# Kernel tuning notes

Measured on AMD Instinct MI355X. Metric: run time of the kernel, lower is better.

The kernel has to match this reference:

```python
import jax, jax.numpy as jnp
import numpy as np

B, C, N, K = 8, 256, 16384, 128  # batch, channels, points per cloud, clusters per cloud


def setup_inputs() -> dict:
    key = jax.random.key(0)
    k1, k2 = jax.random.split(key)
    point_features = jax.random.normal(k1, (B, C, N), dtype=jnp.float32)
    # labels in [-1, K): -1 = noise (skipped by the reduce)
    cluster_ids = jax.random.randint(k2, (B, N), 0, K + 1).astype(jnp.int32) - 1
    return {"point_features": point_features, "cluster_ids": cluster_ids}


def reference(point_features, cluster_ids):
    """Faithful vectorized form of SegHead.forward (eval mode: dropout p=0.3 is identity).

    The torch code loops over (pc, unique cluster label) and does a max over each
    ragged segment. With dense labels 0..K-1 this is exactly a segment-max over
    global segment id pc*K + label; label -1 points are routed to a dump segment.
    """
    b_idx = jnp.arange(B, dtype=cluster_ids.dtype)[:, None]                 # (B,1)
    seg = jnp.where(cluster_ids >= 0, b_idx * K + cluster_ids, B * K)       # (B,N)
    feats = point_features.transpose(0, 2, 1).reshape(B * N, C)             # (B*N, C)
    seg_max = jax.ops.segment_max(feats, seg.reshape(-1), num_segments=B * K + 1)
    all_seg_feats = seg_max[: B * K]                                        # (B*K, C)
    # guard vacuously-empty segments (-inf) -> 0, keeps shapes static under jit
    all_seg_feats = jnp.where(jnp.isfinite(all_seg_feats), all_seg_feats, 0.0)
    # point_features permuted + flattened, as the module writes back
    pf_flat = point_features.transpose(0, 2, 1).reshape(-1, C)              # (B*N, C)
    return all_seg_feats, pf_flat
```

## Files before the change

### kernel.cpp

```cpp
#include <hip/hip_runtime.h>
#include <stdint.h>

#define B_ 8
#define C_ 256
#define N_ 16384
#define K_ 128

#define CT 64
#define PT 1024
#define SUB 64
#define NSUB (PT / SUB)
#define TPAD 65

__device__ __forceinline__ unsigned f2key(float f) {
    unsigned u = __float_as_uint(f);
    return (u & 0x80000000u) ? ~u : (u | 0x80000000u);
}
__device__ __forceinline__ float key2f(unsigned k) {
    unsigned u = (k & 0x80000000u) ? (k & 0x7fffffffu) : ~k;
    return __uint_as_float(u);
}

__global__ __launch_bounds__(256, 2) void seghead_fused(
    const float* __restrict__ pf,
    const int* __restrict__ cid,
    unsigned* __restrict__ gacc,
    float* __restrict__ out1)
{
    __shared__ float tile[CT][TPAD];
    __shared__ unsigned acc[K_ * CT];
    __shared__ int cids[PT];

    const int t = threadIdx.x;
    const int b = blockIdx.z;
    const int c0 = blockIdx.y * CT;
    const int n0 = blockIdx.x * PT;

    for (int i = t; i < K_ * CT; i += 256) acc[i] = 0u;
    for (int i = t; i < PT; i += 256) cids[i] = cid[b * N_ + n0 + i];
    __syncthreads();

    const int x4   = t & 15;
    const int cy   = t >> 4;
    const int lane = t & 63;
    const int w    = t >> 6;

    for (int s = 0; s < NSUB; ++s) {
        const int nb = n0 + s * SUB;

        const float* src = pf + ((size_t)b * C_ + c0) * N_ + nb;
        #pragma unroll
        for (int r = 0; r < 4; ++r) {
            const int c = r * 16 + cy;
            float4 v = *(const float4*)(src + (size_t)c * N_ + x4 * 4);
            tile[c][x4 * 4 + 0] = v.x;
            tile[c][x4 * 4 + 1] = v.y;
            tile[c][x4 * 4 + 2] = v.z;
            tile[c][x4 * 4 + 3] = v.w;
        }
        __syncthreads();

        #pragma unroll
        for (int q = 0; q < 16; ++q) {
            const int nl = w * 16 + q;
            const float v = tile[lane][nl];
            out1[((size_t)b * N_ + nb + nl) * C_ + c0 + lane] = v;
            const int cc = cids[s * SUB + nl];
            if (cc >= 0) atomicMax(&acc[cc * CT + lane], f2key(v));
        }
        __syncthreads();
    }

    for (int i = t; i < K_ * CT; i += 256) {
        const unsigned k = acc[i];
        if (k) {
            const int cl = i >> 6;
            const int ch = i & (CT - 1);
            atomicMax(&gacc[(size_t)(b * K_ + cl) * C_ + c0 + ch], k);
        }
    }
}

__global__ void seghead_finalize(unsigned* __restrict__ gacc) {
    const int i = blockIdx.x * 256 + threadIdx.x;
    const unsigned k = gacc[i];
    ((float*)gacc)[i] = k ? key2f(k) : 0.0f;
}

extern "C" void kernel_launch(void* const* d_in, const int* in_sizes, int n_in,
                              void* d_out, int out_size, void* d_ws, size_t ws_size,
                              hipStream_t stream) {
    const float* pf  = (const float*)d_in[0];
    const int*   cid = (const int*)d_in[1];

    float*    out  = (float*)d_out;
    unsigned* gacc = (unsigned*)d_out;
    float*    out1 = out + (size_t)B_ * K_ * C_;

    hipMemsetAsync(d_out, 0, (size_t)B_ * K_ * C_ * sizeof(unsigned), stream);

    dim3 grid(N_ / PT, C_ / CT, B_);
    seghead_fused<<<grid, 256, 0, stream>>>(pf, cid, gacc, out1);

    seghead_finalize<<<(B_ * K_ * C_) / 256, 256, 0, stream>>>(gacc);
}
```

Baseline: 261.1 us.

## Double-buffer tiles, shrink channel tile, stage atomics at load, reduce partials via workspace

Halves the channel tile to 32 so each block uses less LDS and more blocks fit per CU. Adds a double-buffered shared tile with register prefetch of the next sub-tile, and moves the shared atomicMax into the staging step, using a padded [channel][cluster] accumulator. The transposed output is now written as float4. When the workspace is large enough, per-block partial maxima go to the workspace and a separate kernel reduces them deterministically, which removes the global atomics and the memset at the cost of extra workspace traffic.

```diff
diff --git a/kernel.cpp b/kernel.cpp
--- a/kernel.cpp
+++ b/kernel.cpp
@@ -6,11 +6,15 @@
 #define N_ 16384
 #define K_ 128
 
-#define CT 64
+#define CT 32
 #define PT 1024
 #define SUB 64
 #define NSUB (PT / SUB)
-#define TPAD 65
+#define XBLKS (N_ / PT)
+#define YBLKS (C_ / CT)
+#define ACC_ENTRIES (CT * K_)
+#define NBLOCKS (XBLKS * YBLKS * B_)
+#define WS_BYTES ((size_t)NBLOCKS * ACC_ENTRIES * 4u)
 
 __device__ __forceinline__ unsigned f2key(float f) {
     unsigned u = __float_as_uint(f);
@@ -21,67 +25,109 @@
     return __uint_as_float(u);
 }
 
-__global__ __launch_bounds__(256, 2) void seghead_fused(
+__global__ __launch_bounds__(256, 4) void seghead_fused(
     const float* __restrict__ pf,
     const int* __restrict__ cid,
-    unsigned* __restrict__ gacc,
-    float* __restrict__ out1)
+    float* __restrict__ out1,
+    unsigned* __restrict__ pws,
+    unsigned* __restrict__ gacc)
 {
-    __shared__ float tile[CT][TPAD];
-    __shared__ unsigned acc[K_ * CT];
-    __shared__ int cids[PT];
+    __shared__ float tile[2][CT][SUB + 1];
+    __shared__ unsigned acc[CT][K_ + 1];
 
-    const int t = threadIdx.x;
-    const int b = blockIdx.z;
-    const int c0 = blockIdx.y * CT;
-    const int n0 = blockIdx.x * PT;
+    const int t  = threadIdx.x;
+    const int xb = blockIdx.x, yb = blockIdx.y, b = blockIdx.z;
+    const int c0 = yb * CT;
+    const int n0 = xb * PT;
 
-    for (int i = t; i < K_ * CT; i += 256) acc[i] = 0u;
-    for (int i = t; i < PT; i += 256) cids[i] = cid[b * N_ + n0 + i];
+    for (int i = t; i < CT * (K_ + 1); i += 256) ((unsigned*)acc)[i] = 0u;
+
+    const int x4 = t & 15;
+    const int cy = t >> 4;
+    const float* src0 = pf + ((size_t)(b * C_ + c0 + cy) * N_) + n0 + x4 * 4;
+    const int*   csrc = cid + (size_t)b * N_ + n0 + x4 * 4;
+
+    auto gload = [&](int r, int s) -> float4 {
+        return *(const float4*)(src0 + (size_t)r * 16 * N_ + s * SUB);
+    };
+    auto cload = [&](int s) -> int4 {
+        return *(const int4*)(csrc + s * SUB);
+    };
+    auto stage = [&](int nb, float4 v0, float4 v1, int4 cc) {
+        float* row0 = &tile[nb][cy][x4 * 4];
+        float* row1 = &tile[nb][16 + cy][x4 * 4];
+        row0[0] = v0.x; row0[1] = v0.y; row0[2] = v0.z; row0[3] = v0.w;
+        row1[0] = v1.x; row1[1] = v1.y; row1[2] = v1.z; row1[3] = v1.w;
+        if (cc.x >= 0) { atomicMax(&acc[cy][cc.x], f2key(v0.x)); atomicMax(&acc[16 + cy][cc.x], f2key(v1.x)); }
+        if (cc.y >= 0) { atomicMax(&acc[cy][cc.y], f2key(v0.y)); atomicMax(&acc[16 + cy][cc.y], f2key(v1.y)); }
+        if (cc.z >= 0) { atomicMax(&acc[cy][cc.z], f2key(v0.z)); atomicMax(&acc[16 + cy][cc.z], f2key(v1.z)); }
+        if (cc.w >= 0) { atomicMax(&acc[cy][cc.w], f2key(v0.w)); atomicMax(&acc[16 + cy][cc.w], f2key(v1.w)); }
+    };
+
+    const int lane = t & 63;
+    const int w    = t >> 6;
+    const int g4   = (lane & 7) * 4;
+    const int pp   = lane >> 3;
+    auto process = [&](int nb, int s) {
+        #pragma unroll
+        for (int it = 0; it < 2; ++it) {
+            const int p = w * 16 + it * 8 + pp;
+            float4 o;
+            o.x = tile[nb][g4 + 0][p];
+            o.y = tile[nb][g4 + 1][p];
+            o.z = tile[nb][g4 + 2][p];
+            o.w = tile[nb][g4 + 3][p];
+            *(float4*)&out1[((size_t)b * N_ + n0 + s * SUB + p) * C_ + c0 + g4] = o;
+        }
+    };
+
+    {
+        float4 v0 = gload(0, 0), v1 = gload(1, 0);
+        int4 cc = cload(0);
+        stage(0, v0, v1, cc);
+    }
     __syncthreads();
 
-    const int x4   = t & 15;
-    const int cy   = t >> 4;
-    const int lane = t & 63;
-    const int w    = t >> 6;
-
+    int nb = 0;
     for (int s = 0; s < NSUB; ++s) {
-        const int nb = n0 + s * SUB;
-
-        const float* src = pf + ((size_t)b * C_ + c0) * N_ + nb;
-        #pragma unroll
-        for (int r = 0; r < 4; ++r) {
-            const int c = r * 16 + cy;
-            float4 v = *(const float4*)(src + (size_t)c * N_ + x4 * 4);
-            tile[c][x4 * 4 + 0] = v.x;
-            tile[c][x4 * 4 + 1] = v.y;
-            tile[c][x4 * 4 + 2] = v.z;
-            tile[c][x4 * 4 + 3] = v.w;
-        }
+        float4 v0, v1; int4 cc;
+        const bool more = (s + 1 < NSUB);
+        if (more) { v0 = gload(0, s + 1); v1 = gload(1, s + 1); cc = cload(s + 1); }
+        process(nb, s);
+        if (more) stage(nb ^ 1, v0, v1, cc);
         __syncthreads();
-
-        #pragma unroll
-        for (int q = 0; q < 16; ++q) {
-            const int nl = w * 16 + q;
-            const float v = tile[lane][nl];
-            out1[((size_t)b * N_ + nb + nl) * C_ + c0 + lane] = v;
-            const int cc = cids[s * SUB + nl];
-            if (cc >= 0) atomicMax(&acc[cc * CT + lane], f2key(v));
-        }
-        __syncthreads();
+        nb ^= 1;
     }
 
-    for (int i = t; i < K_ * CT; i += 256) {
-        const unsigned k = acc[i];
-        if (k) {
-            const int cl = i >> 6;
-            const int ch = i & (CT - 1);
-            atomicMax(&gacc[(size_t)(b * K_ + cl) * C_ + c0 + ch], k);
+    const int blin = (b * YBLKS + yb) * XBLKS + xb;
+    if (pws) {
+        unsigned* dst = pws + (size_t)blin * ACC_ENTRIES;
+        for (int i = t; i < ACC_ENTRIES; i += 256)
+            dst[i] = acc[i >> 7][i & 127];
+    } else {
+        for (int i = t; i < ACC_ENTRIES; i += 256) {
+            const unsigned k = acc[i >> 7][i & 127];
+            if (k) atomicMax(&gacc[((size_t)b * K_ + (i & 127)) * C_ + c0 + (i >> 7)], k);
         }
     }
 }
 
-__global__ void seghead_finalize(unsigned* __restrict__ gacc) {
+__global__ void seghead_reduce_ws(const unsigned* __restrict__ pws,
+                                  float* __restrict__ out0) {
+    const int tid  = blockIdx.x * 256 + threadIdx.x;
+    const int cl   = tid & 127;
+    const int rest = tid >> 7;
+    const int c    = rest & 255;
+    const int b    = rest >> 8;
+    const unsigned* p = pws + (size_t)(b * YBLKS + (c >> 5)) * XBLKS * ACC_ENTRIES
+                            + (c & 31) * K_ + cl;
+    unsigned m = 0;
+    #pragma unroll
+    for (int x = 0; x < XBLKS; ++x) m = max(m, p[(size_t)x * ACC_ENTRIES]);
+    out0[((size_t)b * K_ + cl) * C_ + c] = m ? key2f(m) : 0.0f;
+}
+
+__global__ void seghead_decode(unsigned* __restrict__ gacc) {
     const int i = blockIdx.x * 256 + threadIdx.x;
     const unsigned k = gacc[i];
     ((float*)gacc)[i] = k ? key2f(k) : 0.0f;
@@ -90,17 +136,20 @@
 extern "C" void kernel_launch(void* const* d_in, const int* in_sizes, int n_in,
                               void* d_out, int out_size, void* d_ws, size_t ws_size,
                               hipStream_t stream) {
-    const float* pf  = (const float*)d_in[0];
-    const int*   cid = (const int*)d_in[1];
+    const float* pf   = (const float*)d_in[0];
+    const int*   cidp = (const int*)d_in[1];
 
-    float*    out  = (float*)d_out;
-    unsigned* gacc = (unsigned*)d_out;
-    float*    out1 = out + (size_t)B_ * K_ * C_;
+    float* out0 = (float*)d_out;
+    float* out1 = out0 + (size_t)B_ * K_ * C_;
 
-    hipMemsetAsync(d_out, 0, (size_t)B_ * K_ * C_ * sizeof(unsigned), stream);
-
-    dim3 grid(N_ / PT, C_ / CT, B_);
-    seghead_fused<<<grid, 256, 0, stream>>>(pf, cid, gacc, out1);
-
-    seghead_finalize<<<(B_ * K_ * C_) / 256, 256, 0, stream>>>(gacc);
+    dim3 grid(XBLKS, YBLKS, B_);
+    if (ws_size >= WS_BYTES) {
+        unsigned* pws = (unsigned*)d_ws;
+        seghead_fused<<<grid, 256, 0, stream>>>(pf, cidp, out1, pws, nullptr);
+        seghead_reduce_ws<<<(B_ * K_ * C_) / 256, 256, 0, stream>>>(pws, out0);
+    } else {
+        hipMemsetAsync(d_out, 0, (size_t)B_ * K_ * C_ * 4, stream);
+        seghead_fused<<<grid, 256, 0, stream>>>(pf, cidp, out1, nullptr, (unsigned*)d_out);
+        seghead_decode<<<(B_ * K_ * C_) / 256, 256, 0, stream>>>((unsigned*)d_out);
+    }
 }
```

Result: slower. 267.6 us (+2.5%).
